# Performance work log

Hardware: AMD Instinct MI355X
Metric: run time of the kernel (lower is better)

## Reference

```python
import jax, jax.numpy as jnp
import numpy as np

FEATURE_DIM = 512
NUM_NODES = 50
NUM_GCN_LAYERS = 2
H_IMG = W_IMG = 256


def setup_inputs() -> dict:
    key = jax.random.key(0)
    ks = jax.random.split(key, 14)
    s = lambda k, shape: (jax.random.normal(k, shape, jnp.float32) * 0.02)
    return {
        "fts": jax.random.normal(ks[0], (1, FEATURE_DIM, H_IMG, W_IMG), jnp.float32),
        "msk": jax.random.randint(ks[1], (1, H_IMG, W_IMG), 0, 2, jnp.int32),
        "gcn_w": s(ks[2], (NUM_GCN_LAYERS, FEATURE_DIM, FEATURE_DIM)),
        "gcn_b": s(ks[3], (NUM_GCN_LAYERS, FEATURE_DIM)),
        "q_w": s(ks[4], (FEATURE_DIM // 2, FEATURE_DIM)),
        "q_b": s(ks[5], (FEATURE_DIM // 2,)),
        "k_w": s(ks[6], (FEATURE_DIM // 2, FEATURE_DIM)),
        "k_b": s(ks[7], (FEATURE_DIM // 2,)),
        "v_w": s(ks[8], (FEATURE_DIM, FEATURE_DIM)),
        "v_b": s(ks[9], (FEATURE_DIM,)),
        "map_w": s(ks[10], (FEATURE_DIM, FEATURE_DIM)),
        "map_b": s(ks[11], (FEATURE_DIM,)),
        "gamma": jnp.float32(0.1),   # torch inits to 0; nonzero for coverage
        "alpha": jnp.float32(-4.0),  # matches torch init
    }


def _adaptive_avg_pool1d(x, n):
    """torch.nn.AdaptiveAvgPool1d over last axis. x: [C, L] -> [C, n].
    Bin i averages x[:, floor(i*L/n) : ceil((i+1)*L/n)]. Done via cumsum."""
    L = x.shape[-1]
    i = np.arange(n)
    starts = (i * L) // n
    ends = ((i + 1) * L + n - 1) // n  # ceil
    cs = jnp.concatenate([jnp.zeros(x.shape[:-1] + (1,), x.dtype), jnp.cumsum(x, axis=-1)], axis=-1)
    sums = cs[..., ends] - cs[..., starts]
    return sums / jnp.asarray(ends - starts, x.dtype)


def reference(fts, msk, gcn_w, gcn_b, q_w, q_b, k_w, k_b, v_w, v_b, map_w, map_b, gamma, alpha):
    # interpolate(fts, size=msk.shape[-2:]) is identity: sizes already match.
    msk_f = msk.astype(fts.dtype)                     # [1, H, W]
    m = msk_f[:, None]                                # [1, 1, H, W]
    glob_proto = jnp.sum(fts * m, axis=(-2, -1)) / (jnp.sum(msk_f) + 1e-8)  # [1, 512]

    # masked_select -> [512, L] foreground pixels (eager nonzero; msk is data)
    fg_idx = jnp.nonzero(msk.reshape(-1))[0]
    fg = fts.reshape(FEATURE_DIM, -1)[:, fg_idx]      # [512, L]
    local_protos = _adaptive_avg_pool1d(fg, NUM_NODES).T  # [50, 512]

    H = jnp.concatenate([glob_proto, local_protos], axis=0)  # [51, 512]
    for l in range(NUM_GCN_LAYERS):
        Hn = H / jnp.maximum(jnp.linalg.norm(H, axis=1, keepdims=True), 1e-12)
        adj = jax.nn.softmax(jnp.maximum(Hn @ Hn.T, 0.0), axis=1)  # [51, 51]
        agg = adj @ H
        H = H + jax.nn.relu(agg @ gcn_w[l].T + gcn_b[l])

    # cross-attention: q from node 0, k/v from remaining 50 nodes
    q_node, k_nodes = H[:1], H[1:]
    q = q_node @ q_w.T + q_b                          # [1, 256]
    k = k_nodes @ k_w.T + k_b                         # [50, 256]
    v = k_nodes @ v_w.T + v_b                         # [50, 512]
    attn = jax.nn.softmax((q @ k.T) / (q_w.shape[0] ** 0.5), axis=-1)
    final_proto = q_node + gamma * ((attn @ v) @ map_w.T + map_b)  # [1, 512]

    w = jax.nn.sigmoid(alpha)
    return glob_proto * (1 - w) + final_proto * w
```

## Files before the change

### kernel.cpp

```cpp
#include <hip/hip_runtime.h>

#define HW 65536
#define CDIM 512
#define NN 50
#define NROWS 51

__device__ __forceinline__ float wave_sum(float v) {
#pragma unroll
  for (int off = 32; off; off >>= 1) v += __shfl_xor(v, off, 64);
  return v;
}
__device__ __forceinline__ int wave_sum_i(int v) {
#pragma unroll
  for (int off = 32; off; off >>= 1) v += __shfl_xor(v, off, 64);
  return v;
}
__device__ __forceinline__ float wave_max(float v) {
#pragma unroll
  for (int off = 32; off; off >>= 1) v = fmaxf(v, __shfl_xor(v, off, 64));
  return v;
}
__device__ __forceinline__ int wave_max_i(int v) {
#pragma unroll
  for (int off = 32; off; off >>= 1) v = max(v, __shfl_xor(v, off, 64));
  return v;
}
__device__ __forceinline__ int wave_min_i(int v) {
#pragma unroll
  for (int off = 32; off; off >>= 1) v = min(v, __shfl_xor(v, off, 64));
  return v;
}

__global__ __launch_bounds__(256) void k_prep(
    const int* __restrict__ msk, int* __restrict__ blkcnt, float* __restrict__ seg,
    float* __restrict__ nsqB, float* __restrict__ nsqC,
    const float* __restrict__ g0, const float* __restrict__ g1,
    const float* __restrict__ qw, const float* __restrict__ kw,
    const float* __restrict__ vw, const float* __restrict__ mw,
    float* __restrict__ g0T, float* __restrict__ g1T, float* __restrict__ qwT,
    float* __restrict__ kwT, float* __restrict__ vwT, float* __restrict__ mwT) {
  int t = threadIdx.x, b = blockIdx.x;
  __shared__ float tile[32][33];
  __shared__ int wl[4];
  if (b < 64) {
    int g = b * 256 + t;
    if (g < NN * CDIM) seg[g] = 0.f;
    int g2 = g + 16384;
    if (g2 < NN * CDIM) seg[g2] = 0.f;
    if (b == 0 && t < NROWS) { nsqB[t] = 0.f; nsqC[t] = 0.f; }
    int4 m = ((const int4*)msk)[g];
    int c = (m.x != 0) + (m.y != 0) + (m.z != 0) + (m.w != 0);
    c = wave_sum_i(c);
    if ((t & 63) == 0) wl[t >> 6] = c;
    __syncthreads();
    if (t == 0) blkcnt[b] = wl[0] + wl[1] + wl[2] + wl[3];
  } else {
    int tid = b - 64;
    const float* in; float* out; int rows, cols, lt;
    if (tid < 256)       { in = g0; out = g0T; rows = 512; cols = 512; lt = tid; }
    else if (tid < 512)  { in = g1; out = g1T; rows = 512; cols = 512; lt = tid - 256; }
    else if (tid < 640)  { in = qw; out = qwT; rows = 256; cols = 512; lt = tid - 512; }
    else if (tid < 768)  { in = kw; out = kwT; rows = 256; cols = 512; lt = tid - 640; }
    else if (tid < 1024) { in = vw; out = vwT; rows = 512; cols = 512; lt = tid - 768; }
    else                 { in = mw; out = mwT; rows = 512; cols = 512; lt = tid - 1024; }
    int ctiles = cols / 32;
    int r0 = (lt / ctiles) * 32, c0 = (lt % ctiles) * 32;
    int tx = t & 31, ty = t >> 5;
#pragma unroll
    for (int j = 0; j < 4; ++j)
      tile[ty + j * 8][tx] = in[(size_t)(r0 + ty + j * 8) * cols + c0 + tx];
    __syncthreads();
#pragma unroll
    for (int j = 0; j < 4; ++j)
      out[(size_t)(c0 + ty + j * 8) * rows + r0 + tx] = tile[tx][ty + j * 8];
  }
}

__global__ __launch_bounds__(256) void k_rank(const int* __restrict__ msk,
                                              const int* __restrict__ blkcnt,
                                              int* __restrict__ meta,
                                              unsigned char* __restrict__ bin8,
                                              int* __restrict__ P) {
  int t = threadIdx.x, blk = blockIdx.x;
  __shared__ int sblkoff, sL;
  __shared__ int sst[NN + 1];
  __shared__ int wtot[4];
  if (t < 64) {
    int c = blkcnt[t];
    int x = c;
#pragma unroll
    for (int d = 1; d < 64; d <<= 1) {
      int y = __shfl_up(x, d, 64);
      if (t >= d) x += y;
    }
    if (t == blk) sblkoff = x - c;
    if (t == 63) sL = x;
  }
  __syncthreads();
  int L = sL;
  if (t <= NN) sst[t] = (int)((long long)t * L / NN);
  if (blk == 0 && t < NN) {
    if (t == 0) meta[0] = L;
    long long Ll = L;
    int s = (int)((long long)t * Ll / NN);
    int e = (int)(((long long)(t + 1) * Ll + NN - 1) / NN);
    int ci = (int)(((long long)t * Ll + NN - 1) / NN);
    meta[2 + NN + t] = e - s;
    meta[2 + 2 * NN + t] = (t >= 1 && ci > s) ? 1 : 0;
  }
  int4 m = ((const int4*)msk)[blk * 256 + t];
  int fl[4] = {m.x != 0, m.y != 0, m.z != 0, m.w != 0};
  int cnt = fl[0] + fl[1] + fl[2] + fl[3];
  int lane = t & 63, wv = t >> 6;
  int x = cnt;
#pragma unroll
  for (int d = 1; d < 64; d <<= 1) {
    int y = __shfl_up(x, d, 64);
    if (lane >= d) x += y;
  }
  if (lane == 63) wtot[wv] = x;
  __syncthreads();
  int base = sblkoff + (x - cnt);
  for (int w = 0; w < wv; ++w) base += wtot[w];
  int p0 = blk * 1024 + t * 4;
  int r = base;
#pragma unroll
  for (int j = 0; j < 4; ++j) {
    int p = p0 + j;
    unsigned char bv = 255;
    if (fl[j]) {
      int bi = (int)((long long)NN * r / L);
      bv = (unsigned char)bi;
      if (sst[bi] == r) P[bi] = p;
      if (bi + 1 < NN && sst[bi + 1] == r) P[bi + 1] = p;
      r++;
    }
    bin8[p] = bv;
  }
}

__global__ __launch_bounds__(256) void k_seg(const float* __restrict__ fts,
                                             const unsigned char* __restrict__ bin8,
                                             float* __restrict__ seg) {
  int pb = blockIdx.x * 256;
  int t = threadIdx.x, lane = t & 63, wv = t >> 6;
  int cw = blockIdx.y * 64 + wv * 16;
  uchar4 b4 = *(const uchar4*)(bin8 + pb + lane * 4);
  int bb[4] = {b4.x, b4.y, b4.z, b4.w};
  int mn = 255, mx = -1;
#pragma unroll
  for (int j = 0; j < 4; ++j)
    if (bb[j] != 255) { mn = min(mn, bb[j]); mx = max(mx, bb[j]); }
  mn = wave_min_i(mn);
  mx = wave_max_i(mx);
  if (mx < 0) return;
  const float* base = fts + (size_t)cw * HW + pb + lane * 4;
  int span = mx - mn;
  if (span <= 3) {
    int br0 = bb[0] - mn, br1 = bb[1] - mn, br2 = bb[2] - mn, br3 = bb[3] - mn;
    float racc[16][4];
#pragma unroll
    for (int a = 0; a < 16; ++a)
#pragma unroll
      for (int j = 0; j < 4; ++j) racc[a][j] = 0.f;
#pragma unroll 8
    for (int cs = 0; cs < 16; ++cs) {
      float4 v = *(const float4*)(base + (size_t)cs * HW);
      racc[cs][0] += (br0 == 0 ? v.x : 0.f) + (br1 == 0 ? v.y : 0.f) +
                     (br2 == 0 ? v.z : 0.f) + (br3 == 0 ? v.w : 0.f);
      racc[cs][1] += (br0 == 1 ? v.x : 0.f) + (br1 == 1 ? v.y : 0.f) +
                     (br2 == 1 ? v.z : 0.f) + (br3 == 1 ? v.w : 0.f);
      racc[cs][2] += (br0 == 2 ? v.x : 0.f) + (br1 == 2 ? v.y : 0.f) +
                     (br2 == 2 ? v.z : 0.f) + (br3 == 2 ? v.w : 0.f);
      racc[cs][3] += (br0 == 3 ? v.x : 0.f) + (br1 == 3 ? v.y : 0.f) +
                     (br2 == 3 ? v.z : 0.f) + (br3 == 3 ? v.w : 0.f);
    }
#pragma unroll 1
    for (int cs = 0; cs < 16; ++cs) {
#pragma unroll
      for (int j = 0; j < 4; ++j) {
        if (j <= span) {
          float s = wave_sum(racc[cs][j]);
          if (lane == 0 && s != 0.f) atomicAdd(&seg[(mn + j) * CDIM + cw + cs], s);
        }
      }
    }
  } else {
#pragma unroll 1
    for (int cs = 0; cs < 16; ++cs) {
      float4 v = *(const float4*)(base + (size_t)cs * HW);
      float vs[4] = {v.x, v.y, v.z, v.w};
#pragma unroll
      for (int j = 0; j < 4; ++j)
        if (bb[j] != 255) atomicAdd(&seg[bb[j] * CDIM + cw + cs], vs[j]);
    }
  }
}

__global__ __launch_bounds__(512) void k_buildH(const float* __restrict__ fts,
                                                const float* __restrict__ seg,
                                                const int* __restrict__ meta,
                                                const int* __restrict__ P,
                                                float* __restrict__ glob,
                                                float* __restrict__ H,
                                                float* __restrict__ nsq) {
  int r = blockIdx.x, c = threadIdx.x;
  int L = meta[0];
  float h;
  if (r == 0) {
    float s = 0.f;
#pragma unroll 5
    for (int i = 0; i < NN; ++i) s += seg[i * CDIM + c];
    h = s / ((float)L + 1e-8f);
    glob[c] = h;
  } else {
    int i = r - 1;
    float s = seg[i * CDIM + c];
    if (meta[2 + 2 * NN + i]) s += fts[(size_t)c * HW + P[i]];
    h = s / fmaxf((float)meta[2 + NN + i], 1.f);
  }
  H[r * CDIM + c] = h;
  float x = wave_sum(h * h);
  __shared__ float wsum[8];
  if ((c & 63) == 0) wsum[c >> 6] = x;
  __syncthreads();
  if (c == 0) {
    float s = 0.f;
#pragma unroll
    for (int w = 0; w < 8; ++w) s += wsum[w];
    nsq[r] = s;
  }
}

__global__ __launch_bounds__(128) void k_gcn(const float* __restrict__ Hin,
                                             const float* __restrict__ nsqIn,
                                             float* __restrict__ Hout,
                                             float* __restrict__ nsqOut,
                                             const float* __restrict__ WT,
                                             const float* __restrict__ bias) {
  int a = blockIdx.x, s = blockIdx.y;
  int t = threadIdx.x, lane = t & 63, w = t >> 6;
  __shared__ float sHa[CDIM];
  __shared__ float sadj[64];
  __shared__ float sagg[CDIM];
#pragma unroll
  for (int i = 0; i < 4; ++i) sHa[t + i * 128] = Hin[a * CDIM + t + i * 128];
  __syncthreads();
  float na = fmaxf(sqrtf(nsqIn[a]), 1e-12f);
  for (int b = w; b < NROWS; b += 2) {
    float d = 0.f;
    const float* hb = Hin + b * CDIM;
#pragma unroll
    for (int k = 0; k < 8; ++k) d += sHa[lane + k * 64] * hb[lane + k * 64];
    d = wave_sum(d);
    if (lane == 0) {
      float nb = fmaxf(sqrtf(nsqIn[b]), 1e-12f);
      sadj[b] = fmaxf(d / (na * nb), 0.f);
    }
  }
  __syncthreads();
  if (t < 64) {
    float sv = (t < NROWS) ? sadj[t] : -1e30f;
    float m = wave_max(sv);
    float e = (t < NROWS) ? expf(sv - m) : 0.f;
    float sum = wave_sum(e);
    if (t < NROWS) sadj[t] = e / sum;
  }
  __syncthreads();
#pragma unroll
  for (int ci = 0; ci < 4; ++ci) {
    int c = t + ci * 128;
    float acc = 0.f;
#pragma unroll 3
    for (int b = 0; b < NROWS; ++b) acc += sadj[b] * Hin[b * CDIM + c];
    sagg[c] = acc;
  }
  __syncthreads();
  int c = s * 128 + t;
  float acc = bias[c];
#pragma unroll 16
  for (int k = 0; k < CDIM; ++k) acc += sagg[k] * WT[k * CDIM + c];
  float h = sHa[c] + fmaxf(acc, 0.f);
  Hout[a * CDIM + c] = h;
  float p = wave_sum(h * h);
  if (lane == 0) atomicAdd(&nsqOut[a], p);
}

__global__ __launch_bounds__(128) void k_qkv(const float* __restrict__ H,
                                             const float* __restrict__ qwT,
                                             const float* __restrict__ kwT,
                                             const float* __restrict__ vwT,
                                             const float* __restrict__ qb,
                                             const float* __restrict__ kb,
                                             const float* __restrict__ vb,
                                             float* __restrict__ q,
                                             float* __restrict__ kk,
                                             float* __restrict__ vv) {
  int a = blockIdx.x, s = blockIdx.y, t = threadIdx.x;
  __shared__ float sh[CDIM];
#pragma unroll
  for (int i = 0; i < 4; ++i) sh[t + i * 128] = H[a * CDIM + t + i * 128];
  __syncthreads();
  if (a == 0) {
    if (t < 64) {
      int c = s * 64 + t;
      float acc = qb[c];
#pragma unroll 16
      for (int k = 0; k < CDIM; ++k) acc += sh[k] * qwT[k * 256 + c];
      q[c] = acc;
    }
  } else {
    int i = a - 1;
    if (t < 64) {
      int c = s * 64 + t;
      float acc = kb[c];
#pragma unroll 16
      for (int k = 0; k < CDIM; ++k) acc += sh[k] * kwT[k * 256 + c];
      kk[i * 256 + c] = acc;
    }
    int c = s * 128 + t;
    float acc = vb[c];
#pragma unroll 16
    for (int k = 0; k < CDIM; ++k) acc += sh[k] * vwT[k * CDIM + c];
    vv[i * CDIM + c] = acc;
  }
}

__global__ __launch_bounds__(128) void k_final(const float* __restrict__ H,
                                               const float* __restrict__ glob,
                                               const float* __restrict__ q,
                                               const float* __restrict__ kk,
                                               const float* __restrict__ vv,
                                               const float* __restrict__ mwT,
                                               const float* __restrict__ mapb,
                                               const float* __restrict__ gamma,
                                               const float* __restrict__ alpha,
                                               float* __restrict__ out) {
  int t = threadIdx.x, lane = t & 63, w = t >> 6;
  __shared__ float sattn[64];
  __shared__ float sav[CDIM];
  for (int i = w; i < NN; i += 2) {
    float d = 0.f;
#pragma unroll
    for (int k = 0; k < 4; ++k) d += q[lane + k * 64] * kk[i * 256 + lane + k * 64];
    d = wave_sum(d);
    if (lane == 0) sattn[i] = d * (1.f / 16.f);
  }
  __syncthreads();
  if (t < 64) {
    float sv = (t < NN) ? sattn[t] : -1e30f;
    float m = wave_max(sv);
    float e = (t < NN) ? expf(sv - m) : 0.f;
    float sum = wave_sum(e);
    if (t < NN) sattn[t] = e / sum;
  }
  __syncthreads();
#pragma unroll
  for (int ci = 0; ci < 4; ++ci) {
    int c = t + ci * 128;
    float acc = 0.f;
#pragma unroll 5
    for (int i = 0; i < NN; ++i) acc += sattn[i] * vv[i * CDIM + c];
    sav[c] = acc;
  }
  __syncthreads();
  int c = blockIdx.x * 128 + t;
  float o = mapb[c];
#pragma unroll 16
  for (int k = 0; k < CDIM; ++k) o += sav[k] * mwT[k * CDIM + c];
  float wv_ = 1.f / (1.f + expf(-alpha[0]));
  float fp = H[c] + gamma[0] * o;
  out[c] = glob[c] * (1.f - wv_) + fp * wv_;
}

extern "C" void kernel_launch(void* const* d_in, const int* in_sizes, int n_in,
                              void* d_out, int out_size, void* d_ws, size_t ws_size,
                              hipStream_t stream) {
  const float* fts = (const float*)d_in[0];
  const int* msk = (const int*)d_in[1];
  const float* gcn_w = (const float*)d_in[2];
  const float* gcn_b = (const float*)d_in[3];
  const float* q_w = (const float*)d_in[4];
  const float* q_b = (const float*)d_in[5];
  const float* k_w = (const float*)d_in[6];
  const float* k_b = (const float*)d_in[7];
  const float* v_w = (const float*)d_in[8];
  const float* v_b = (const float*)d_in[9];
  const float* map_w = (const float*)d_in[10];
  const float* map_b = (const float*)d_in[11];
  const float* gamma = (const float*)d_in[12];
  const float* alpha = (const float*)d_in[13];
  float* out = (float*)d_out;

  char* wp = (char*)d_ws;
  auto alloc = [&](size_t bytes) {
    char* p = wp;
    wp += (bytes + 255) & ~(size_t)255;
    return p;
  };
  float* g0T = (float*)alloc(512 * 512 * 4);
  float* g1T = (float*)alloc(512 * 512 * 4);
  float* qwT = (float*)alloc(512 * 256 * 4);
  float* kwT = (float*)alloc(512 * 256 * 4);
  float* vwT = (float*)alloc(512 * 512 * 4);
  float* mwT = (float*)alloc(512 * 512 * 4);
  int* blkcnt = (int*)alloc(64 * 4);
  int* meta = (int*)alloc(160 * 4);
  int* P = (int*)alloc(NN * 4);
  unsigned char* bin8 = (unsigned char*)alloc(HW);
  float* seg = (float*)alloc(NN * CDIM * 4);
  float* glob = (float*)alloc(CDIM * 4);
  float* HA = (float*)alloc(NROWS * CDIM * 4);
  float* HB = (float*)alloc(NROWS * CDIM * 4);
  float* HC = (float*)alloc(NROWS * CDIM * 4);
  float* nsqA = (float*)alloc(NROWS * 4);
  float* nsqB = (float*)alloc(NROWS * 4);
  float* nsqC = (float*)alloc(NROWS * 4);
  float* qv = (float*)alloc(256 * 4);
  float* kv = (float*)alloc(NN * 256 * 4);
  float* vv = (float*)alloc(NN * CDIM * 4);

  k_prep<<<1344, 256, 0, stream>>>(msk, blkcnt, seg, nsqB, nsqC,
                                   gcn_w, gcn_w + 512 * 512, q_w, k_w, v_w, map_w,
                                   g0T, g1T, qwT, kwT, vwT, mwT);
  k_rank<<<64, 256, 0, stream>>>(msk, blkcnt, meta, bin8, P);
  k_seg<<<dim3(256, 8), 256, 0, stream>>>(fts, bin8, seg);
  k_buildH<<<NROWS, 512, 0, stream>>>(fts, seg, meta, P, glob, HA, nsqA);
  k_gcn<<<dim3(NROWS, 4), 128, 0, stream>>>(HA, nsqA, HB, nsqB, g0T, gcn_b);
  k_gcn<<<dim3(NROWS, 4), 128, 0, stream>>>(HB, nsqB, HC, nsqC, g1T, gcn_b + 512);
  k_qkv<<<dim3(NROWS, 4), 128, 0, stream>>>(HC, qwT, kwT, vwT, q_b, k_b, v_b, qv, kv, vv);
  k_final<<<4, 128, 0, stream>>>(HC, glob, qv, kv, vv, mwT, map_b, gamma, alpha, out);
}
```

Before: 454.2 us.

## Fuse GCN, QKV and final stages into one persistent kernel with grid barriers

Merges buildH, both GCN layers, QKV projection and the final attention into one 51-block kernel that synchronises through atomic grid barriers. The weight transposes move from the prep kernel into this tail kernel. The segment-sum kernel now has each block cover 512 pixels instead of 256, and its fast path is limited to spans of at most 2 bins using mask multiplies. The goal is to remove launch overhead and inter-kernel gaps in the tail. In exchange, the tail runs on only 51 blocks, so the matvecs get less parallelism, and the spin barriers rely on all blocks being co-resident.

After: 465.1 us. +2.4%, slower.

```diff
diff --git a/kernel.cpp b/kernel.cpp
--- a/kernel.cpp
+++ b/kernel.cpp
@@ -31,49 +31,23 @@
   return v;
 }
 
-__global__ __launch_bounds__(256) void k_prep(
-    const int* __restrict__ msk, int* __restrict__ blkcnt, float* __restrict__ seg,
-    float* __restrict__ nsqB, float* __restrict__ nsqC,
-    const float* __restrict__ g0, const float* __restrict__ g1,
-    const float* __restrict__ qw, const float* __restrict__ kw,
-    const float* __restrict__ vw, const float* __restrict__ mw,
-    float* __restrict__ g0T, float* __restrict__ g1T, float* __restrict__ qwT,
-    float* __restrict__ kwT, float* __restrict__ vwT, float* __restrict__ mwT) {
+__global__ __launch_bounds__(256) void k_prep(const int* __restrict__ msk,
+                                              int* __restrict__ blkcnt,
+                                              float* __restrict__ seg,
+                                              int* __restrict__ bar) {
   int t = threadIdx.x, b = blockIdx.x;
-  __shared__ float tile[32][33];
+  int g = b * 256 + t;
+  if (g < NN * CDIM) seg[g] = 0.f;
+  int g2 = g + 16384;
+  if (g2 < NN * CDIM) seg[g2] = 0.f;
+  if (b == 0 && t < 8) bar[t] = 0;
+  int4 m = ((const int4*)msk)[g];
+  int c = (m.x != 0) + (m.y != 0) + (m.z != 0) + (m.w != 0);
+  c = wave_sum_i(c);
   __shared__ int wl[4];
-  if (b < 64) {
-    int g = b * 256 + t;
-    if (g < NN * CDIM) seg[g] = 0.f;
-    int g2 = g + 16384;
-    if (g2 < NN * CDIM) seg[g2] = 0.f;
-    if (b == 0 && t < NROWS) { nsqB[t] = 0.f; nsqC[t] = 0.f; }
-    int4 m = ((const int4*)msk)[g];
-    int c = (m.x != 0) + (m.y != 0) + (m.z != 0) + (m.w != 0);
-    c = wave_sum_i(c);
-    if ((t & 63) == 0) wl[t >> 6] = c;
-    __syncthreads();
-    if (t == 0) blkcnt[b] = wl[0] + wl[1] + wl[2] + wl[3];
-  } else {
-    int tid = b - 64;
-    const float* in; float* out; int rows, cols, lt;
-    if (tid < 256)       { in = g0; out = g0T; rows = 512; cols = 512; lt = tid; }
-    else if (tid < 512)  { in = g1; out = g1T; rows = 512; cols = 512; lt = tid - 256; }
-    else if (tid < 640)  { in = qw; out = qwT; rows = 256; cols = 512; lt = tid - 512; }
-    else if (tid < 768)  { in = kw; out = kwT; rows = 256; cols = 512; lt = tid - 640; }
-    else if (tid < 1024) { in = vw; out = vwT; rows = 512; cols = 512; lt = tid - 768; }
-    else                 { in = mw; out = mwT; rows = 512; cols = 512; lt = tid - 1024; }
-    int ctiles = cols / 32;
-    int r0 = (lt / ctiles) * 32, c0 = (lt % ctiles) * 32;
-    int tx = t & 31, ty = t >> 5;
-#pragma unroll
-    for (int j = 0; j < 4; ++j)
-      tile[ty + j * 8][tx] = in[(size_t)(r0 + ty + j * 8) * cols + c0 + tx];
-    __syncthreads();
-#pragma unroll
-    for (int j = 0; j < 4; ++j)
-      out[(size_t)(c0 + ty + j * 8) * rows + r0 + tx] = tile[tx][ty + j * 8];
-  }
+  if ((t & 63) == 0) wl[t >> 6] = c;
+  __syncthreads();
+  if (t == 0) blkcnt[b] = wl[0] + wl[1] + wl[2] + wl[3];
 }
 
 __global__ __launch_bounds__(256) void k_rank(const int* __restrict__ msk,
@@ -142,235 +116,284 @@
 __global__ __launch_bounds__(256) void k_seg(const float* __restrict__ fts,
                                              const unsigned char* __restrict__ bin8,
                                              float* __restrict__ seg) {
-  int pb = blockIdx.x * 256;
+  int pb = blockIdx.x * 512;
   int t = threadIdx.x, lane = t & 63, wv = t >> 6;
   int cw = blockIdx.y * 64 + wv * 16;
-  uchar4 b4 = *(const uchar4*)(bin8 + pb + lane * 4);
-  int bb[4] = {b4.x, b4.y, b4.z, b4.w};
+  uchar4 u0 = *(const uchar4*)(bin8 + pb + lane * 4);
+  uchar4 u1 = *(const uchar4*)(bin8 + pb + 256 + lane * 4);
+  int bb[8] = {u0.x, u0.y, u0.z, u0.w, u1.x, u1.y, u1.z, u1.w};
   int mn = 255, mx = -1;
 #pragma unroll
-  for (int j = 0; j < 4; ++j)
+  for (int j = 0; j < 8; ++j)
     if (bb[j] != 255) { mn = min(mn, bb[j]); mx = max(mx, bb[j]); }
   mn = wave_min_i(mn);
   mx = wave_max_i(mx);
   if (mx < 0) return;
+  int span = mx - mn;
   const float* base = fts + (size_t)cw * HW + pb + lane * 4;
-  int span = mx - mn;
-  if (span <= 3) {
-    int br0 = bb[0] - mn, br1 = bb[1] - mn, br2 = bb[2] - mn, br3 = bb[3] - mn;
-    float racc[16][4];
-#pragma unroll
-    for (int a = 0; a < 16; ++a)
-#pragma unroll
-      for (int j = 0; j < 4; ++j) racc[a][j] = 0.f;
-#pragma unroll 8
-    for (int cs = 0; cs < 16; ++cs) {
-      float4 v = *(const float4*)(base + (size_t)cs * HW);
-      racc[cs][0] += (br0 == 0 ? v.x : 0.f) + (br1 == 0 ? v.y : 0.f) +
-                     (br2 == 0 ? v.z : 0.f) + (br3 == 0 ? v.w : 0.f);
-      racc[cs][1] += (br0 == 1 ? v.x : 0.f) + (br1 == 1 ? v.y : 0.f) +
-                     (br2 == 1 ? v.z : 0.f) + (br3 == 1 ? v.w : 0.f);
-      racc[cs][2] += (br0 == 2 ? v.x : 0.f) + (br1 == 2 ? v.y : 0.f) +
-                     (br2 == 2 ? v.z : 0.f) + (br3 == 2 ? v.w : 0.f);
-      racc[cs][3] += (br0 == 3 ? v.x : 0.f) + (br1 == 3 ? v.y : 0.f) +
-                     (br2 == 3 ? v.z : 0.f) + (br3 == 3 ? v.w : 0.f);
+  if (span <= 1) {
+    float mlo[8], mhi[8];
+#pragma unroll
+    for (int j = 0; j < 8; ++j) {
+      mlo[j] = (bb[j] == mn) ? 1.f : 0.f;
+      mhi[j] = (bb[j] == mx) ? 1.f : 0.f;
+    }
+    float alo[16], ahi[16];
+#pragma unroll
+    for (int cs = 0; cs < 16; ++cs) { alo[cs] = 0.f; ahi[cs] = 0.f; }
+    if (span == 0) {
+#pragma unroll 4
+      for (int cs = 0; cs < 16; ++cs) {
+        const float* p = base + (size_t)cs * HW;
+        float4 v0 = *(const float4*)p;
+        float4 v1 = *(const float4*)(p + 256);
+        alo[cs] = v0.x * mlo[0] + v0.y * mlo[1] + v0.z * mlo[2] + v0.w * mlo[3] +
+                  v1.x * mlo[4] + v1.y * mlo[5] + v1.z * mlo[6] + v1.w * mlo[7];
+      }
+    } else {
+#pragma unroll 4
+      for (int cs = 0; cs < 16; ++cs) {
+        const float* p = base + (size_t)cs * HW;
+        float4 v0 = *(const float4*)p;
+        float4 v1 = *(const float4*)(p + 256);
+        alo[cs] = v0.x * mlo[0] + v0.y * mlo[1] + v0.z * mlo[2] + v0.w * mlo[3] +
+                  v1.x * mlo[4] + v1.y * mlo[5] + v1.z * mlo[6] + v1.w * mlo[7];
+        ahi[cs] = v0.x * mhi[0] + v0.y * mhi[1] + v0.z * mhi[2] + v0.w * mhi[3] +
+                  v1.x * mhi[4] + v1.y * mhi[5] + v1.z * mhi[6] + v1.w * mhi[7];
+      }
     }
 #pragma unroll 1
     for (int cs = 0; cs < 16; ++cs) {
-#pragma unroll
-      for (int j = 0; j < 4; ++j) {
-        if (j <= span) {
-          float s = wave_sum(racc[cs][j]);
-          if (lane == 0 && s != 0.f) atomicAdd(&seg[(mn + j) * CDIM + cw + cs], s);
-        }
+      float s = wave_sum(alo[cs]);
+      if (lane == 0 && s != 0.f) atomicAdd(&seg[mn * CDIM + cw + cs], s);
+    }
+    if (span == 1) {
+#pragma unroll 1
+      for (int cs = 0; cs < 16; ++cs) {
+        float s = wave_sum(ahi[cs]);
+        if (lane == 0 && s != 0.f) atomicAdd(&seg[mx * CDIM + cw + cs], s);
       }
     }
   } else {
 #pragma unroll 1
     for (int cs = 0; cs < 16; ++cs) {
-      float4 v = *(const float4*)(base + (size_t)cs * HW);
-      float vs[4] = {v.x, v.y, v.z, v.w};
-#pragma unroll
-      for (int j = 0; j < 4; ++j)
+      const float* p = base + (size_t)cs * HW;
+      float4 v0 = *(const float4*)p;
+      float4 v1 = *(const float4*)(p + 256);
+      float vs[8] = {v0.x, v0.y, v0.z, v0.w, v1.x, v1.y, v1.z, v1.w};
+#pragma unroll
+      for (int j = 0; j < 8; ++j)
         if (bb[j] != 255) atomicAdd(&seg[bb[j] * CDIM + cw + cs], vs[j]);
     }
   }
 }
 
-__global__ __launch_bounds__(512) void k_buildH(const float* __restrict__ fts,
-                                                const float* __restrict__ seg,
-                                                const int* __restrict__ meta,
-                                                const int* __restrict__ P,
-                                                float* __restrict__ glob,
-                                                float* __restrict__ H,
-                                                float* __restrict__ nsq) {
-  int r = blockIdx.x, c = threadIdx.x;
-  int L = meta[0];
-  float h;
-  if (r == 0) {
-    float s = 0.f;
+__device__ __forceinline__ void gbar(int* bar, int id, int nblk) {
+  __syncthreads();
+  if (threadIdx.x == 0) {
+    __hip_atomic_fetch_add(&bar[id], 1, __ATOMIC_ACQ_REL, __HIP_MEMORY_SCOPE_AGENT);
+    while (__hip_atomic_load(&bar[id], __ATOMIC_ACQUIRE, __HIP_MEMORY_SCOPE_AGENT) < nblk)
+      __builtin_amdgcn_s_sleep(4);
+  }
+  __syncthreads();
+}
+
+__global__ __launch_bounds__(256) void k_tail(
+    const float* __restrict__ fts, const float* __restrict__ seg,
+    const int* __restrict__ meta, const int* __restrict__ P,
+    const float* __restrict__ g0, const float* __restrict__ g1,
+    const float* __restrict__ qw, const float* __restrict__ kw,
+    const float* __restrict__ vw, const float* __restrict__ mw,
+    const float* __restrict__ gcn_b,
+    const float* __restrict__ qb, const float* __restrict__ kb,
+    const float* __restrict__ vb, const float* __restrict__ mapb,
+    const float* __restrict__ gamma, const float* __restrict__ alpha,
+    float* __restrict__ g0T, float* __restrict__ g1T, float* __restrict__ qwT,
+    float* __restrict__ kwT, float* __restrict__ vwT, float* __restrict__ mwT,
+    float* __restrict__ glob, float* __restrict__ HA, float* __restrict__ HB,
+    float* __restrict__ HC, float* __restrict__ nsqA, float* __restrict__ nsqB,
+    float* __restrict__ qv, float* __restrict__ kv, float* __restrict__ vv,
+    float* __restrict__ out, int* __restrict__ bar) {
+  int r = blockIdx.x;
+  int t = threadIdx.x, lane = t & 63, w = t >> 6;
+  __shared__ float tile[32][33];
+  __shared__ float sHa[CDIM];
+  __shared__ float sagg[CDIM];
+  __shared__ float sadj[64];
+  __shared__ float wsum[4];
+
+  for (int tid = r; tid < 1280; tid += NROWS) {
+    const float* in; float* outp; int rows, cols, lt;
+    if (tid < 256)       { in = g0; outp = g0T; rows = 512; cols = 512; lt = tid; }
+    else if (tid < 512)  { in = g1; outp = g1T; rows = 512; cols = 512; lt = tid - 256; }
+    else if (tid < 640)  { in = qw; outp = qwT; rows = 256; cols = 512; lt = tid - 512; }
+    else if (tid < 768)  { in = kw; outp = kwT; rows = 256; cols = 512; lt = tid - 640; }
+    else if (tid < 1024) { in = vw; outp = vwT; rows = 512; cols = 512; lt = tid - 768; }
+    else                 { in = mw; outp = mwT; rows = 512; cols = 512; lt = tid - 1024; }
+    int ctiles = cols / 32;
+    int r0 = (lt / ctiles) * 32, c0 = (lt % ctiles) * 32;
+    int tx = t & 31, ty = t >> 5;
+#pragma unroll
+    for (int j = 0; j < 4; ++j)
+      tile[ty + j * 8][tx] = in[(size_t)(r0 + ty + j * 8) * cols + c0 + tx];
+    __syncthreads();
+#pragma unroll
+    for (int j = 0; j < 4; ++j)
+      outp[(size_t)(c0 + ty + j * 8) * rows + r0 + tx] = tile[tx][ty + j * 8];
+    __syncthreads();
+  }
+
+  {
+    int L = meta[0];
+    float nl = 0.f;
+#pragma unroll
+    for (int half = 0; half < 2; ++half) {
+      int c = t + half * 256;
+      float h;
+      if (r == 0) {
+        float s = 0.f;
 #pragma unroll 5
-    for (int i = 0; i < NN; ++i) s += seg[i * CDIM + c];
-    h = s / ((float)L + 1e-8f);
-    glob[c] = h;
-  } else {
-    int i = r - 1;
-    float s = seg[i * CDIM + c];
-    if (meta[2 + 2 * NN + i]) s += fts[(size_t)c * HW + P[i]];
-    h = s / fmaxf((float)meta[2 + NN + i], 1.f);
-  }
-  H[r * CDIM + c] = h;
-  float x = wave_sum(h * h);
-  __shared__ float wsum[8];
-  if ((c & 63) == 0) wsum[c >> 6] = x;
-  __syncthreads();
-  if (c == 0) {
-    float s = 0.f;
-#pragma unroll
-    for (int w = 0; w < 8; ++w) s += wsum[w];
-    nsq[r] = s;
-  }
-}
-
-__global__ __launch_bounds__(128) void k_gcn(const float* __restrict__ Hin,
-                                             const float* __restrict__ nsqIn,
-                                             float* __restrict__ Hout,
-                                             float* __restrict__ nsqOut,
-                                             const float* __restrict__ WT,
-                                             const float* __restrict__ bias) {
-  int a = blockIdx.x, s = blockIdx.y;
-  int t = threadIdx.x, lane = t & 63, w = t >> 6;
-  __shared__ float sHa[CDIM];
-  __shared__ float sadj[64];
-  __shared__ float sagg[CDIM];
-#pragma unroll
-  for (int i = 0; i < 4; ++i) sHa[t + i * 128] = Hin[a * CDIM + t + i * 128];
-  __syncthreads();
-  float na = fmaxf(sqrtf(nsqIn[a]), 1e-12f);
-  for (int b = w; b < NROWS; b += 2) {
+        for (int i = 0; i < NN; ++i) s += seg[i * CDIM + c];
+        h = s / ((float)L + 1e-8f);
+        glob[c] = h;
+      } else {
+        int i = r - 1;
+        float s = seg[i * CDIM + c];
+        if (meta[2 + 2 * NN + i]) s += fts[(size_t)c * HW + P[i]];
+        h = s / fmaxf((float)meta[2 + NN + i], 1.f);
+      }
+      HA[r * CDIM + c] = h;
+      nl += h * h;
+    }
+    nl = wave_sum(nl);
+    if (lane == 0) wsum[w] = nl;
+    __syncthreads();
+    if (t == 0) nsqA[r] = wsum[0] + wsum[1] + wsum[2] + wsum[3];
+  }
+  gbar(bar, 0, NROWS);
+
+#pragma unroll 1
+  for (int l = 0; l < 2; ++l) {
+    const float* Hin = l ? HB : HA;
+    float* Hout = l ? HC : HB;
+    const float* nsq = l ? nsqB : nsqA;
+    float* nsqOut = l ? nsqA : nsqB;
+    const float* WT = l ? g1T : g0T;
+    const float* bias = gcn_b + l * CDIM;
+    sHa[t] = Hin[r * CDIM + t];
+    sHa[t + 256] = Hin[r * CDIM + t + 256];
+    __syncthreads();
+    float na = fmaxf(sqrtf(nsq[r]), 1e-12f);
+    for (int b = w; b < NROWS; b += 4) {
+      const float* hb = Hin + b * CDIM;
+      float d = 0.f;
+#pragma unroll
+      for (int k = 0; k < 8; ++k) d += sHa[lane + k * 64] * hb[lane + k * 64];
+      d = wave_sum(d);
+      if (lane == 0) {
+        float nb = fmaxf(sqrtf(nsq[b]), 1e-12f);
+        sadj[b] = fmaxf(d / (na * nb), 0.f);
+      }
+    }
+    __syncthreads();
+    if (t < 64) {
+      float sv = (t < NROWS) ? sadj[t] : -1e30f;
+      float m = wave_max(sv);
+      float e = (t < NROWS) ? expf(sv - m) : 0.f;
+      float su = wave_sum(e);
+      if (t < NROWS) sadj[t] = e / su;
+    }
+    __syncthreads();
+#pragma unroll
+    for (int half = 0; half < 2; ++half) {
+      int c = t + half * 256;
+      float acc = 0.f;
+#pragma unroll 3
+      for (int b = 0; b < NROWS; ++b) acc += sadj[b] * Hin[b * CDIM + c];
+      sagg[c] = acc;
+    }
+    __syncthreads();
+    float nl = 0.f;
+#pragma unroll
+    for (int half = 0; half < 2; ++half) {
+      int c = t + half * 256;
+      float acc = bias[c];
+#pragma unroll 8
+      for (int k = 0; k < CDIM; ++k) acc += sagg[k] * WT[k * CDIM + c];
+      float h = sHa[c] + fmaxf(acc, 0.f);
+      Hout[r * CDIM + c] = h;
+      nl += h * h;
+    }
+    nl = wave_sum(nl);
+    if (lane == 0) wsum[w] = nl;
+    __syncthreads();
+    if (t == 0) nsqOut[r] = wsum[0] + wsum[1] + wsum[2] + wsum[3];
+    gbar(bar, 1 + l, NROWS);
+  }
+
+  {
+    sHa[t] = HC[r * CDIM + t];
+    sHa[t + 256] = HC[r * CDIM + t + 256];
+    __syncthreads();
+    if (r == 0) {
+      float acc = qb[t];
+#pragma unroll 8
+      for (int k = 0; k < CDIM; ++k) acc += sHa[k] * qwT[k * 256 + t];
+      qv[t] = acc;
+    } else {
+      int i = r - 1;
+      float acc = kb[t];
+#pragma unroll 8
+      for (int k = 0; k < CDIM; ++k) acc += sHa[k] * kwT[k * 256 + t];
+      kv[i * 256 + t] = acc;
+      float a0 = vb[t], a1 = vb[t + 256];
+#pragma unroll 8
+      for (int k = 0; k < CDIM; ++k) {
+        float hv = sHa[k];
+        a0 += hv * vwT[k * CDIM + t];
+        a1 += hv * vwT[k * CDIM + t + 256];
+      }
+      vv[i * CDIM + t] = a0;
+      vv[i * CDIM + t + 256] = a1;
+    }
+  }
+  gbar(bar, 3, NROWS);
+  if (r >= 4) return;
+
+  for (int i = w; i < NN; i += 4) {
     float d = 0.f;
-    const float* hb = Hin + b * CDIM;
-#pragma unroll
-    for (int k = 0; k < 8; ++k) d += sHa[lane + k * 64] * hb[lane + k * 64];
+#pragma unroll
+    for (int k = 0; k < 4; ++k) d += qv[lane + k * 64] * kv[i * 256 + lane + k * 64];
     d = wave_sum(d);
-    if (lane == 0) {
-      float nb = fmaxf(sqrtf(nsqIn[b]), 1e-12f);
-      sadj[b] = fmaxf(d / (na * nb), 0.f);
-    }
+    if (lane == 0) sadj[i] = d * (1.f / 16.f);
   }
   __syncthreads();
   if (t < 64) {
-    float sv = (t < NROWS) ? sadj[t] : -1e30f;
-    float m = wave_max(sv);
-    float e = (t < NROWS) ? expf(sv - m) : 0.f;
-    float sum = wave_sum(e);
-    if (t < NROWS) sadj[t] = e / sum;
-  }
-  __syncthreads();
-#pragma unroll
-  for (int ci = 0; ci < 4; ++ci) {
-    int c = t + ci * 128;
-    float acc = 0.f;
-#pragma unroll 3
-    for (int b = 0; b < NROWS; ++b) acc += sadj[b] * Hin[b * CDIM + c];
-    sagg[c] = acc;
-  }
-  __syncthreads();
-  int c = s * 128 + t;
-  float acc = bias[c];
-#pragma unroll 16
-  for (int k = 0; k < CDIM; ++k) acc += sagg[k] * WT[k * CDIM + c];
-  float h = sHa[c] + fmaxf(acc, 0.f);
-  Hout[a * CDIM + c] = h;
-  float p = wave_sum(h * h);
-  if (lane == 0) atomicAdd(&nsqOut[a], p);
-}
-
-__global__ __launch_bounds__(128) void k_qkv(const float* __restrict__ H,
-                                             const float* __restrict__ qwT,
-                                             const float* __restrict__ kwT,
-                                             const float* __restrict__ vwT,
-                                             const float* __restrict__ qb,
-                                             const float* __restrict__ kb,
-                                             const float* __restrict__ vb,
-                                             float* __restrict__ q,
-                                             float* __restrict__ kk,
-                                             float* __restrict__ vv) {
-  int a = blockIdx.x, s = blockIdx.y, t = threadIdx.x;
-  __shared__ float sh[CDIM];
-#pragma unroll
-  for (int i = 0; i < 4; ++i) sh[t + i * 128] = H[a * CDIM + t + i * 128];
-  __syncthreads();
-  if (a == 0) {
-    if (t < 64) {
-      int c = s * 64 + t;
-      float acc = qb[c];
-#pragma unroll 16
-      for (int k = 0; k < CDIM; ++k) acc += sh[k] * qwT[k * 256 + c];
-      q[c] = acc;
-    }
-  } else {
-    int i = a - 1;
-    if (t < 64) {
-      int c = s * 64 + t;
-      float acc = kb[c];
-#pragma unroll 16
-      for (int k = 0; k < CDIM; ++k) acc += sh[k] * kwT[k * 256 + c];
-      kk[i * 256 + c] = acc;
-    }
-    int c = s * 128 + t;
-    float acc = vb[c];
-#pragma unroll 16
-    for (int k = 0; k < CDIM; ++k) acc += sh[k] * vwT[k * CDIM + c];
-    vv[i * CDIM + c] = acc;
-  }
-}
-
-__global__ __launch_bounds__(128) void k_final(const float* __restrict__ H,
-                                               const float* __restrict__ glob,
-                                               const float* __restrict__ q,
-                                               const float* __restrict__ kk,
-                                               const float* __restrict__ vv,
-                                               const float* __restrict__ mwT,
-                                               const float* __restrict__ mapb,
-                                               const float* __restrict__ gamma,
-                                               const float* __restrict__ alpha,
-                                               float* __restrict__ out) {
-  int t = threadIdx.x, lane = t & 63, w = t >> 6;
-  __shared__ float sattn[64];
-  __shared__ float sav[CDIM];
-  for (int i = w; i < NN; i += 2) {
-    float d = 0.f;
-#pragma unroll
-    for (int k = 0; k < 4; ++k) d += q[lane + k * 64] * kk[i * 256 + lane + k * 64];
-    d = wave_sum(d);
-    if (lane == 0) sattn[i] = d * (1.f / 16.f);
-  }
-  __syncthreads();
-  if (t < 64) {
-    float sv = (t < NN) ? sattn[t] : -1e30f;
+    float sv = (t < NN) ? sadj[t] : -1e30f;
     float m = wave_max(sv);
     float e = (t < NN) ? expf(sv - m) : 0.f;
-    float sum = wave_sum(e);
-    if (t < NN) sattn[t] = e / sum;
-  }
-  __syncthreads();
-#pragma unroll
-  for (int ci = 0; ci < 4; ++ci) {
-    int c = t + ci * 128;
+    float su = wave_sum(e);
+    if (t < NN) sadj[t] = e / su;
+  }
+  __syncthreads();
+#pragma unroll
+  for (int half = 0; half < 2; ++half) {
+    int c = t + half * 256;
     float acc = 0.f;
 #pragma unroll 5
-    for (int i = 0; i < NN; ++i) acc += sattn[i] * vv[i * CDIM + c];
-    sav[c] = acc;
-  }
-  __syncthreads();
-  int c = blockIdx.x * 128 + t;
-  float o = mapb[c];
-#pragma unroll 16
-  for (int k = 0; k < CDIM; ++k) o += sav[k] * mwT[k * CDIM + c];
-  float wv_ = 1.f / (1.f + expf(-alpha[0]));
-  float fp = H[c] + gamma[0] * o;
-  out[c] = glob[c] * (1.f - wv_) + fp * wv_;
+    for (int i = 0; i < NN; ++i) acc += sadj[i] * vv[i * CDIM + c];
+    sagg[c] = acc;
+  }
+  __syncthreads();
+  if (t < 128) {
+    int c = r * 128 + t;
+    float o = mapb[c];
+#pragma unroll 8
+    for (int k = 0; k < CDIM; ++k) o += sagg[k] * mwT[k * CDIM + c];
+    float wv_ = 1.f / (1.f + expf(-alpha[0]));
+    float fp = HC[c] + gamma[0] * o;
+    out[c] = glob[c] * (1.f - wv_) + fp * wv_;
+  }
 }
 
 extern "C" void kernel_launch(void* const* d_in, const int* in_sizes, int n_in,
@@ -415,19 +438,17 @@
   float* HC = (float*)alloc(NROWS * CDIM * 4);
   float* nsqA = (float*)alloc(NROWS * 4);
   float* nsqB = (float*)alloc(NROWS * 4);
-  float* nsqC = (float*)alloc(NROWS * 4);
   float* qv = (float*)alloc(256 * 4);
   float* kv = (float*)alloc(NN * 256 * 4);
   float* vv = (float*)alloc(NN * CDIM * 4);
-
-  k_prep<<<1344, 256, 0, stream>>>(msk, blkcnt, seg, nsqB, nsqC,
-                                   gcn_w, gcn_w + 512 * 512, q_w, k_w, v_w, map_w,
-                                   g0T, g1T, qwT, kwT, vwT, mwT);
+  int* bar = (int*)alloc(8 * 4);
+
+  k_prep<<<64, 256, 0, stream>>>(msk, blkcnt, seg, bar);
   k_rank<<<64, 256, 0, stream>>>(msk, blkcnt, meta, bin8, P);
-  k_seg<<<dim3(256, 8), 256, 0, stream>>>(fts, bin8, seg);
-  k_buildH<<<NROWS, 512, 0, stream>>>(fts, seg, meta, P, glob, HA, nsqA);
-  k_gcn<<<dim3(NROWS, 4), 128, 0, stream>>>(HA, nsqA, HB, nsqB, g0T, gcn_b);
-  k_gcn<<<dim3(NROWS, 4), 128, 0, stream>>>(HB, nsqB, HC, nsqC, g1T, gcn_b + 512);
-  k_qkv<<<dim3(NROWS, 4), 128, 0, stream>>>(HC, qwT, kwT, vwT, q_b, k_b, v_b, qv, kv, vv);
-  k_final<<<4, 128, 0, stream>>>(HC, glob, qv, kv, vv, mwT, map_b, gamma, alpha, out);
-}
+  k_seg<<<dim3(128, 8), 256, 0, stream>>>(fts, bin8, seg);
+  k_tail<<<NROWS, 256, 0, stream>>>(
+      fts, seg, meta, P, gcn_w, gcn_w + 512 * 512, q_w, k_w, v_w, map_w,
+      gcn_b, q_b, k_b, v_b, map_b, gamma, alpha,
+      g0T, g1T, qwT, kwT, vwT, mwT, glob, HA, HB, HC, nsqA, nsqB,
+      qv, kv, vv, out, bar);
+}
```
